# Kernel optimization log

Measured on AMD Instinct MI355X. Metric: run time of the kernel, lower is better.

Reference implementation:

```python
import jax, jax.numpy as jnp
import numpy as np

N = 50000        # nodes
E = 1_600_000    # edges
F = 32           # in/out channels
T = 4            # towers
FT = F // T      # per-tower channels = 8
ED = 16          # edge_dim
L = 5            # num PNA layers


def setup_inputs() -> dict:
    key = jax.random.key(0)
    ks = jax.random.split(key, 11)
    s = 0.2  # weight scale
    return {
        "x": jax.random.normal(ks[0], (N, F), jnp.float32),
        "edge_index": jax.random.randint(ks[1], (2, E), 0, N, dtype=jnp.int32),
        "edge_attr": jax.random.normal(ks[2], (E, ED), jnp.float32),
        # per-layer stacked PNAConv parameters
        "edge_W": jax.random.normal(ks[3], (L, ED, FT), jnp.float32) * s,
        "edge_b": jax.random.normal(ks[4], (L, FT), jnp.float32) * s,
        "pre_W": jax.random.normal(ks[5], (L, T, 3 * FT, FT), jnp.float32) * s,
        "pre_b": jax.random.normal(ks[6], (L, T, FT), jnp.float32) * s,
        "post_W": jax.random.normal(ks[7], (L, T, 4 * FT, FT), jnp.float32) * s,
        "post_b": jax.random.normal(ks[8], (L, T, FT), jnp.float32) * s,
        "lin_W": jax.random.normal(ks[9], (L, T * FT, F), jnp.float32) * s,
        "lin_b": jax.random.normal(ks[10], (L, F), jnp.float32) * s,
    }


def _pna_layer(x, src, dst, edge_attr, eW, eb, pW, pb, poW, pob, lW, lb):
    n = x.shape[0]
    xt = x.reshape(n, T, FT)                       # divide_input=True
    ee = edge_attr @ eW + eb                       # [E, FT], shared edge encoder
    xi = xt[dst]                                   # target node features [E, T, FT]
    xj = xt[src]                                   # source node features [E, T, FT]
    ee_b = jnp.broadcast_to(ee[:, None, :], (ee.shape[0], T, FT))
    h = jnp.concatenate([xi, xj, ee_b], axis=-1)   # [E, T, 3*FT]
    # per-tower pre-MLP (pre_layers=1)
    h = jnp.einsum('etk,tkf->etf', h, pW) + pb     # [E, T, FT]
    # aggregators: mean, sum, max (scaler = identity)
    ssum = jax.ops.segment_sum(h, dst, num_segments=n)
    cnt = jax.ops.segment_sum(jnp.ones((h.shape[0],), h.dtype), dst, num_segments=n)
    mean = ssum / jnp.maximum(cnt, 1.0)[:, None, None]
    mx = jax.ops.segment_max(h, dst, num_segments=n)
    mx = jnp.where(cnt[:, None, None] > 0, mx, 0.0)  # empty segments -> 0 (PyG convention)
    out = jnp.concatenate([xt, mean, ssum, mx], axis=-1)  # [N, T, 4*FT]
    # per-tower post-MLP (post_layers=1)
    out = jnp.einsum('ntk,tkf->ntf', out, poW) + pob      # [N, T, FT]
    out = out.reshape(n, T * FT) @ lW + lb                # final mixing linear
    return jax.nn.relu(out)


def reference(x, edge_index, edge_attr, edge_W, edge_b, pre_W, pre_b,
              post_W, post_b, lin_W, lin_b):
    src, dst = edge_index[0], edge_index[1]
    for l in range(L):
        x = _pna_layer(x, src, dst, edge_attr,
                       edge_W[l], edge_b[l], pre_W[l], pre_b[l],
                       post_W[l], post_b[l], lin_W[l], lin_b[l])
    return x
```

## Files before the change

### kernel.cpp

```cpp
#include <hip/hip_runtime.h>
#include <hip/hip_fp16.h>

#define NN 50000
#define NE 1600000
#define F 32
#define T 4
#define FT 8
#define ED 16
#define NLAYERS 5

typedef _Float16 h2 __attribute__((ext_vector_type(2)));

__device__ __forceinline__ float dot2(h2 a, h2 b, float c) {
#if __has_builtin(__builtin_amdgcn_fdot2)
    return __builtin_amdgcn_fdot2(a, b, c, false);
#else
    return c + (float)a.x * (float)b.x + (float)a.y * (float)b.y;
#endif
}

#if __has_builtin(__builtin_amdgcn_global_load_lds)
#define HAS_GLDS 1
__device__ __forceinline__ void glds16(const void* g, void* l) {
    __builtin_amdgcn_global_load_lds(
        (const __attribute__((address_space(1))) unsigned*)g,
        (__attribute__((address_space(3))) unsigned*)l, 16, 0, 0);
}
__device__ __forceinline__ void glds4(const void* g, void* l) {
    __builtin_amdgcn_global_load_lds(
        (const __attribute__((address_space(1))) unsigned*)g,
        (__attribute__((address_space(3))) unsigned*)l, 4, 0, 0);
}
#endif


__global__ void zero_cnt(int* __restrict__ cnt) {
    int i = blockIdx.x * 256 + threadIdx.x;
    if (i < NN) cnt[i] = 0;
}

__global__ void count_kernel(const int* __restrict__ ei, int* __restrict__ cnt) {
    int e = blockIdx.x * 256 + threadIdx.x;
    if (e >= NE) return;
    atomicAdd(&cnt[ei[NE + e]], 1);
}

__global__ void scan_kernel(const int* __restrict__ cnt, int* __restrict__ row_ptr,
                            int* __restrict__ cursor) {
    __shared__ int wsum[16];
    __shared__ int carry_s;
    int tid = threadIdx.x;
    int lane = tid & 63, wid = tid >> 6;
    if (tid == 0) carry_s = 0;
    __syncthreads();
    for (int base = 0; base < NN; base += 1024) {
        int i = base + tid;
        int v = (i < NN) ? cnt[i] : 0;
        int s = v;
#pragma unroll
        for (int off = 1; off < 64; off <<= 1) {
            int tt = __shfl_up(s, off, 64);
            if (lane >= off) s += tt;
        }
        __syncthreads();
        if (lane == 63) wsum[wid] = s;
        __syncthreads();
        if (wid == 0 && lane < 16) {
            int w = wsum[lane];
            int ws = w;
#pragma unroll
            for (int off = 1; off < 16; off <<= 1) {
                int tt = __shfl_up(ws, off, 16);
                if (lane >= off) ws += tt;
            }
            wsum[lane] = ws - w;
        }
        __syncthreads();
        int excl = carry_s + wsum[wid] + s - v;
        if (i < NN) { row_ptr[i] = excl; cursor[i] = excl; }
        __syncthreads();
        if (tid == 1023) carry_s += wsum[15] + s;
    }
}

__global__ void build_kernel(const int* __restrict__ ei,
                             const float* __restrict__ eattr,
                             int* __restrict__ cursor,
                             int* __restrict__ src_s,
                             float4* __restrict__ eh) {
    int e = blockIdx.x * 256 + threadIdx.x;
    if (e >= NE) return;
    int src = ei[e];
    int dst = ei[NE + e];
    const float4* eap = (const float4*)(eattr + (size_t)e * ED);
    float4 v0 = eap[0], v1 = eap[1], v2 = eap[2], v3 = eap[3];
    union { __half hh[16]; float4 f4[2]; } u;
    u.hh[0]  = __float2half(v0.x); u.hh[1]  = __float2half(v0.y);
    u.hh[2]  = __float2half(v0.z); u.hh[3]  = __float2half(v0.w);
    u.hh[4]  = __float2half(v1.x); u.hh[5]  = __float2half(v1.y);
    u.hh[6]  = __float2half(v1.z); u.hh[7]  = __float2half(v1.w);
    u.hh[8]  = __float2half(v2.x); u.hh[9]  = __float2half(v2.y);
    u.hh[10] = __float2half(v2.z); u.hh[11] = __float2half(v2.w);
    u.hh[12] = __float2half(v3.x); u.hh[13] = __float2half(v3.y);
    u.hh[14] = __float2half(v3.z); u.hh[15] = __float2half(v3.w);
    int p = atomicAdd(&cursor[dst], 1);
    src_s[p] = src << 5;
    eh[2 * (size_t)p]     = u.f4[0];
    eh[2 * (size_t)p + 1] = u.f4[1];
}

__global__ void layer_const(const float* __restrict__ edge_W,
                            const float* __restrict__ edge_b,
                            const float* __restrict__ pre_W,
                            const float* __restrict__ pre_b,
                            float4* __restrict__ wchp,
                            float* __restrict__ abias) {
    int idx = threadIdx.x;
    if (idx >= NLAYERS * 32) return;
    int l = idx >> 5, ch = idx & 31;
    int t = ch >> 3, f = ch & 7;
    const float* eW = edge_W + (size_t)l * ED * FT;
    const float* eb = edge_b + (size_t)l * FT;
    const float* pW = pre_W + (size_t)l * T * 24 * FT;
    const float* pb = pre_b + (size_t)l * T * FT;
    float pj[8];
#pragma unroll
    for (int j = 0; j < 8; j++) pj[j] = pW[(t * 24 + 16 + j) * 8 + f];
    union { _Float16 hh[16]; float4 f4[2]; } u;
#pragma unroll
    for (int k = 0; k < 16; k++) {
        float s = 0.f;
#pragma unroll
        for (int j = 0; j < 8; j++) s += eW[k * 8 + j] * pj[j];
        u.hh[k] = (_Float16)s;
    }
    float c0 = pb[t * 8 + f];
#pragma unroll
    for (int j = 0; j < 8; j++) c0 += eb[j] * pj[j];
    wchp[2 * idx]     = u.f4[0];
    wchp[2 * idx + 1] = u.f4[1];
    abias[idx] = c0;
}


__device__ __forceinline__ unsigned short f2bf_rne(float v) {
    unsigned u = __float_as_uint(v);
    return (unsigned short)((u + 0x7FFFu + ((u >> 16) & 1u)) >> 16);
}

__global__ void node_pre(const float* __restrict__ xin,
                         const float* __restrict__ preW,
                         unsigned short* __restrict__ b16) {
    int idx = blockIdx.x * 256 + threadIdx.x;
    if (idx >= NN * F) return;
    int n = idx >> 5, ch = idx & 31;
    int t = ch >> 3, f = ch & 7;
    const float* xrow = xin + n * F + t * FT;
    const float* wB = preW + (t * 24 + 8) * 8 + f;
    float bv = 0.f;
#pragma unroll
    for (int k = 0; k < 8; k++) bv += xrow[k] * wB[k * 8];
    b16[idx] = f2bf_rne(bv);
}

__global__ __launch_bounds__(256) void gather_post(
        const float* __restrict__ xin,
        const unsigned short* __restrict__ b16_in,
        unsigned short* __restrict__ b16_out,
        const float4* __restrict__ eh,
        const int* __restrict__ row_ptr, const int* __restrict__ cnt,
        const int* __restrict__ src_s,
        const float4* __restrict__ wchp_l,
        const float* __restrict__ abias_l,
        const float* __restrict__ preW,
        const float* __restrict__ postW, const float* __restrict__ postb,
        const float* __restrict__ linW, const float* __restrict__ linb,
        const float* __restrict__ preW_next,
        float* __restrict__ xout) {
    __shared__ __align__(16) char stage[4][2304];
    __shared__ float smS[4][32];
    __shared__ float smM[4][32];
    int tid = threadIdx.x;
    int wv = tid >> 6;
    int lane = tid & 63;
    int n = blockIdx.x * 4 + wv;

    int chgrp = lane >> 3;
    int e_sub = lane & 7;
    const unsigned short* bp = b16_in + chgrp * 4;

    union { float4 f4[8]; h2 p[32]; } uw;
#pragma unroll
    for (int c = 0; c < 4; c++) {
        uw.f4[2 * c]     = wchp_l[2 * (chgrp * 4 + c)];
        uw.f4[2 * c + 1] = wchp_l[2 * (chgrp * 4 + c) + 1];
    }

    int rs = row_ptr[n], deg = cnt[n];
    int re = rs + deg;
    float xv = xin[(size_t)n * F + (lane & 31)];

    char* ehbuf = stage[wv];
    const int* srcbuf = (const int*)(stage[wv] + 2048);

    float S[4] = {0.f, 0.f, 0.f, 0.f};
    float M[4] = {-3.4e38f, -3.4e38f, -3.4e38f, -3.4e38f};
    const unsigned MAXS = (NN - 1) * F;

    for (int base = rs; base < re; base += 64) {
        const char* ehb = (const char*)(eh + 2 * (size_t)base);
#ifdef HAS_GLDS
        glds16(ehb + lane * 16, ehbuf);
        glds16(ehb + 1024 + lane * 16, ehbuf + 1024);
        glds4((const char*)(src_s + base) + lane * 4, (void*)srcbuf);
        asm volatile("s_waitcnt vmcnt(0)" ::: "memory");
#else
        *(float4*)(ehbuf + lane * 16) = *(const float4*)(ehb + lane * 16);
        *(float4*)(ehbuf + 1024 + lane * 16) = *(const float4*)(ehb + 1024 + lane * 16);
        ((int*)srcbuf)[lane] = src_s[base + lane];
#endif
        ushort4 bk[8];
#pragma unroll
        for (int k = 0; k < 8; k++) {
            unsigned s = (unsigned)srcbuf[e_sub + 8 * k];
            if (s > MAXS) s = 0;
            bk[k] = *(const ushort4*)(bp + s);
        }
#pragma unroll
        for (int k = 0; k < 8; k++) {
            int j = e_sub + 8 * k;
            bool valid = (base + j) < re;
            union { float4 f4; h2 p[4]; } ua, ub;
            ua.f4 = *(const float4*)(ehbuf + j * 32);
            ub.f4 = *(const float4*)(ehbuf + j * 32 + 16);
            unsigned short bvv[4] = {bk[k].x, bk[k].y, bk[k].z, bk[k].w};
#pragma unroll
            for (int c = 0; c < 4; c++) {
                float h = __uint_as_float((unsigned)bvv[c] << 16);
                h = dot2(ua.p[0], uw.p[c * 8 + 0], h);
                h = dot2(ua.p[1], uw.p[c * 8 + 1], h);
                h = dot2(ua.p[2], uw.p[c * 8 + 2], h);
                h = dot2(ua.p[3], uw.p[c * 8 + 3], h);
                h = dot2(ub.p[0], uw.p[c * 8 + 4], h);
                h = dot2(ub.p[1], uw.p[c * 8 + 5], h);
                h = dot2(ub.p[2], uw.p[c * 8 + 6], h);
                h = dot2(ub.p[3], uw.p[c * 8 + 7], h);
                S[c] += valid ? h : 0.f;
                M[c] = valid ? fmaxf(M[c], h) : M[c];
            }
        }
    }
#pragma unroll
    for (int m = 1; m < 8; m <<= 1) {
#pragma unroll
        for (int c = 0; c < 4; c++) {
            S[c] += __shfl_xor(S[c], m, 64);
            M[c] = fmaxf(M[c], __shfl_xor(M[c], m, 64));
        }
    }
    if (e_sub == 0) {
#pragma unroll
        for (int c = 0; c < 4; c++) {
            smS[wv][chgrp * 4 + c] = S[c];
            smM[wv][chgrp * 4 + c] = M[c];
        }
    }
    __syncthreads();

    int ch = lane & 31, half = lane >> 5;
    int t = ch >> 3, f = ch & 7;
    float Sc = smS[wv][ch];
    float Mc = smM[wv][ch];

    float a_val = abias_l[ch];
#pragma unroll
    for (int j = 0; j < 8; j++)
        a_val += __shfl(xv, t * 8 + j, 64) * preW[(t * 24 + j) * 8 + f];

    float sum_h, mean_h, max_h;
    if (deg > 0) {
        sum_h = Sc + (float)deg * a_val;
        mean_h = sum_h / (float)deg;
        max_h = Mc + a_val;
    } else {
        sum_h = 0.f; mean_h = 0.f; max_h = 0.f;
    }

    float ua0 = 0.f, ua1 = 0.f, ua2 = 0.f, ua3 = 0.f;
#pragma unroll
    for (int kk = 0; kk < 8; kk++) {
        int sl = t * 8 + kk;
        ua0 += __shfl(xv,     sl, 64) * postW[(t * 32 + 0 * 8 + kk) * 8 + f];
        ua1 += __shfl(mean_h, sl, 64) * postW[(t * 32 + 1 * 8 + kk) * 8 + f];
        ua2 += __shfl(sum_h,  sl, 64) * postW[(t * 32 + 2 * 8 + kk) * 8 + f];
        ua3 += __shfl(max_h,  sl, 64) * postW[(t * 32 + 3 * 8 + kk) * 8 + f];
    }
    float u2 = postb[t * 8 + f] + ((ua0 + ua1) + (ua2 + ua3));

    float y0 = 0.f, y1 = 0.f, y2 = 0.f, y3 = 0.f;
#pragma unroll
    for (int k = 0; k < 8; k++) {
        y0 += __shfl(u2, k,      64) * linW[k * 32 + ch];
        y1 += __shfl(u2, 8 + k,  64) * linW[(8 + k) * 32 + ch];
        y2 += __shfl(u2, 16 + k, 64) * linW[(16 + k) * 32 + ch];
        y3 += __shfl(u2, 24 + k, 64) * linW[(24 + k) * 32 + ch];
    }
    float y = linb[ch] + ((y0 + y1) + (y2 + y3));
    y = fmaxf(y, 0.f);
    if (half == 0)
        xout[(size_t)n * F + ch] = y;

    if (preW_next) {
        float bn = 0.f;
#pragma unroll
        for (int j = 0; j < 8; j++)
            bn += __shfl(y, t * 8 + j, 64) * preW_next[(t * 24 + 8 + j) * 8 + f];
        if (half == 0)
            b16_out[(size_t)n * F + ch] = f2bf_rne(bn);
    }
}


extern "C" void kernel_launch(void* const* d_in, const int* in_sizes, int n_in,
                              void* d_out, int out_size, void* d_ws, size_t ws_size,
                              hipStream_t stream) {
    const float* x      = (const float*)d_in[0];
    const int*   ei     = (const int*)d_in[1];
    const float* eattr  = (const float*)d_in[2];
    const float* edge_W = (const float*)d_in[3];
    const float* edge_b = (const float*)d_in[4];
    const float* pre_W  = (const float*)d_in[5];
    const float* pre_b  = (const float*)d_in[6];
    const float* post_W = (const float*)d_in[7];
    const float* post_b = (const float*)d_in[8];
    const float* lin_W  = (const float*)d_in[9];
    const float* lin_b  = (const float*)d_in[10];
    float* out = (float*)d_out;

    const size_t NC = (size_t)NN * F;
    char* p = (char*)d_ws;
    float4* eh    = (float4*)p;        p += sizeof(float4) * 2 * (size_t)NE;
    int* src_s    = (int*)p;           p += sizeof(int) * NE;
    int* cnt      = (int*)p;           p += sizeof(int) * NN;
    int* row_ptr  = (int*)p;           p += sizeof(int) * NN;
    int* cursor   = (int*)p;           p += sizeof(int) * NN;
    unsigned short* b16a = (unsigned short*)p;  p += sizeof(unsigned short) * NC;
    unsigned short* b16b = (unsigned short*)p;  p += sizeof(unsigned short) * NC;
    float* xb0    = (float*)p;         p += sizeof(float) * NC;
    float* xb1    = (float*)p;         p += sizeof(float) * NC;
    float4* wchp  = (float4*)p;        p += sizeof(float4) * 2 * NLAYERS * 32;
    float* abias  = (float*)p;         p += sizeof(float) * NLAYERS * 32;

    dim3 blk(256);
    int gN  = (NN + 255) / 256;
    int gE  = (NE + 255) / 256;
    int gNC = (NN * F + 255) / 256;
    int gG  = NN / 4;

    hipLaunchKernelGGL(zero_cnt,     dim3(gN), blk, 0, stream, cnt);
    hipLaunchKernelGGL(count_kernel, dim3(gE), blk, 0, stream, ei, cnt);
    hipLaunchKernelGGL(scan_kernel,  dim3(1), dim3(1024), 0, stream, cnt, row_ptr, cursor);
    hipLaunchKernelGGL(build_kernel, dim3(gE), blk, 0, stream, ei, eattr,
                       cursor, src_s, eh);
    hipLaunchKernelGGL(layer_const,  dim3(1), blk, 0, stream,
                       edge_W, edge_b, pre_W, pre_b, wchp, abias);

    hipLaunchKernelGGL(node_pre, dim3(gNC), blk, 0, stream, x, pre_W, b16a);

    const float* xin = x;
    for (int l = 0; l < NLAYERS; l++) {
        const float* pW  = pre_W  + (size_t)l * T * 24 * FT;
        const float* poW = post_W + (size_t)l * T * 32 * FT;
        const float* pob = post_b + (size_t)l * T * FT;
        const float* lW  = lin_W  + (size_t)l * F * F;
        const float* lb  = lin_b  + (size_t)l * F;
        const float* pWn = (l + 1 < NLAYERS) ? (pre_W + (size_t)(l + 1) * T * 24 * FT)
                                             : nullptr;
        float* xout = (l == NLAYERS - 1) ? out : ((l & 1) ? xb1 : xb0);
        const unsigned short* bin  = (l & 1) ? b16b : b16a;
        unsigned short*       bout = (l & 1) ? b16a : b16b;

        hipLaunchKernelGGL(gather_post, dim3(gG), blk, 0, stream,
                           xin, bin, pWn ? bout : nullptr, eh, row_ptr, cnt, src_s,
                           wchp + (size_t)l * 64, abias + (size_t)l * 32,
                           pW, poW, pob, lW, lb, pWn, xout);
        xin = xout;
    }
}
```

Measured before the change: 744.9 us.

## Sort nodes by degree, double-buffer edge staging, and narrow lane channel groups

Adds a degree histogram and counting sort so each block's four waves handle nodes of similar degree, which reduces per-block imbalance. The gather loop now processes edges in chunks of 32 with double-buffered async global-to-LDS loads, prefetching the next chunk while the current one is computed. Each lane now covers 2 channels across 4 edge sub-lanes instead of 4 channels across 8, cutting registers and the shuffle-reduction depth. In exchange it adds three small preprocessing kernels, an indirection for node ids, and a scattered write order for outputs.

```diff
diff --git a/kernel.cpp b/kernel.cpp
--- a/kernel.cpp
+++ b/kernel.cpp
@@ -34,9 +34,10 @@
 #endif
 
 
-__global__ void zero_cnt(int* __restrict__ cnt) {
+__global__ void zero_cnt(int* __restrict__ cnt, int* __restrict__ dhist) {
     int i = blockIdx.x * 256 + threadIdx.x;
     if (i < NN) cnt[i] = 0;
+    if (blockIdx.x == 0 && threadIdx.x < 256) dhist[threadIdx.x] = 0;
 }
 
 __global__ void count_kernel(const int* __restrict__ ei, int* __restrict__ cnt) {
@@ -81,6 +82,29 @@
         __syncthreads();
         if (tid == 1023) carry_s += wsum[15] + s;
     }
+}
+
+__global__ void hist_kernel(const int* __restrict__ cnt, int* __restrict__ dhist) {
+    int n = blockIdx.x * 256 + threadIdx.x;
+    if (n >= NN) return;
+    int d = cnt[n]; if (d > 255) d = 255;
+    atomicAdd(&dhist[d], 1);
+}
+
+__global__ void scan_hist(const int* __restrict__ dhist, int* __restrict__ dcur) {
+    if (threadIdx.x == 0) {
+        int acc = 0;
+        for (int i = 0; i < 256; i++) { dcur[i] = acc; acc += dhist[i]; }
+    }
+}
+
+__global__ void order_kernel(const int* __restrict__ cnt, int* __restrict__ dcur,
+                             int* __restrict__ node_order) {
+    int n = blockIdx.x * 256 + threadIdx.x;
+    if (n >= NN) return;
+    int d = cnt[n]; if (d > 255) d = 255;
+    int pos = atomicAdd(&dcur[d], 1);
+    node_order[pos] = n;
 }
 
 __global__ void build_kernel(const int* __restrict__ ei,
@@ -170,6 +194,7 @@
         const float4* __restrict__ eh,
         const int* __restrict__ row_ptr, const int* __restrict__ cnt,
         const int* __restrict__ src_s,
+        const int* __restrict__ node_order,
         const float4* __restrict__ wchp_l,
         const float* __restrict__ abias_l,
         const float* __restrict__ preW,
@@ -183,87 +208,107 @@
     int tid = threadIdx.x;
     int wv = tid >> 6;
     int lane = tid & 63;
-    int n = blockIdx.x * 4 + wv;
-
-    int chgrp = lane >> 3;
-    int e_sub = lane & 7;
-    const unsigned short* bp = b16_in + chgrp * 4;
-
-    union { float4 f4[8]; h2 p[32]; } uw;
-#pragma unroll
-    for (int c = 0; c < 4; c++) {
-        uw.f4[2 * c]     = wchp_l[2 * (chgrp * 4 + c)];
-        uw.f4[2 * c + 1] = wchp_l[2 * (chgrp * 4 + c) + 1];
-    }
+    int n = node_order[blockIdx.x * 4 + wv];
+
+    int chgrp = lane >> 2;
+    int e_sub = lane & 3;
+    const unsigned short* bp = b16_in + chgrp * 2;
+
+    union { float4 f4[4]; h2 p[16]; } uw;
+    uw.f4[0] = wchp_l[2 * (chgrp * 2)];
+    uw.f4[1] = wchp_l[2 * (chgrp * 2) + 1];
+    uw.f4[2] = wchp_l[2 * (chgrp * 2 + 1)];
+    uw.f4[3] = wchp_l[2 * (chgrp * 2 + 1) + 1];
 
     int rs = row_ptr[n], deg = cnt[n];
     int re = rs + deg;
+    int nch = (deg + 31) >> 5;
     float xv = xin[(size_t)n * F + (lane & 31)];
 
-    char* ehbuf = stage[wv];
-    const int* srcbuf = (const int*)(stage[wv] + 2048);
-
-    float S[4] = {0.f, 0.f, 0.f, 0.f};
-    float M[4] = {-3.4e38f, -3.4e38f, -3.4e38f, -3.4e38f};
+    char* stw = stage[wv];
     const unsigned MAXS = (NN - 1) * F;
 
-    for (int base = rs; base < re; base += 64) {
-        const char* ehb = (const char*)(eh + 2 * (size_t)base);
+    float S0 = 0.f, S1 = 0.f, M0 = -3.4e38f, M1 = -3.4e38f;
+
 #ifdef HAS_GLDS
-        glds16(ehb + lane * 16, ehbuf);
-        glds16(ehb + 1024 + lane * 16, ehbuf + 1024);
-        glds4((const char*)(src_s + base) + lane * 4, (void*)srcbuf);
+    {
+        const char* ehg = (const char*)(eh + 2 * (size_t)rs);
+        glds16(ehg + lane * 16, stw);
+        if (lane < 32) glds4((const char*)(src_s + rs) + lane * 4, stw + 2048);
+    }
+    for (int c = 0; c < nch; ++c) {
+        int base = rs + c * 32;
+        const char* eb = stw + (c & 1) * 1024;
+        const int* sb = (const int*)(stw + 2048 + (c & 1) * 128);
         asm volatile("s_waitcnt vmcnt(0)" ::: "memory");
-#else
-        *(float4*)(ehbuf + lane * 16) = *(const float4*)(ehb + lane * 16);
-        *(float4*)(ehbuf + 1024 + lane * 16) = *(const float4*)(ehb + 1024 + lane * 16);
-        ((int*)srcbuf)[lane] = src_s[base + lane];
-#endif
-        ushort4 bk[8];
+        __builtin_amdgcn_sched_barrier(0);
+        ushort2 bk[8];
 #pragma unroll
         for (int k = 0; k < 8; k++) {
-            unsigned s = (unsigned)srcbuf[e_sub + 8 * k];
+            unsigned s = (unsigned)sb[e_sub + 4 * k];
             if (s > MAXS) s = 0;
-            bk[k] = *(const ushort4*)(bp + s);
+            bk[k] = *(const ushort2*)(bp + s);
         }
+        __builtin_amdgcn_sched_barrier(0);
+        int nxt = (c + 1 < nch) ? base + 32 : base;
+        const char* ehgn = (const char*)(eh + 2 * (size_t)nxt);
+        char* ebn = stw + ((c + 1) & 1) * 1024;
+        glds16(ehgn + lane * 16, ebn);
+        if (lane < 32) glds4((const char*)(src_s + nxt) + lane * 4,
+                             stw + 2048 + ((c + 1) & 1) * 128);
+        __builtin_amdgcn_sched_barrier(0);
 #pragma unroll
         for (int k = 0; k < 8; k++) {
-            int j = e_sub + 8 * k;
+            int j = e_sub + 4 * k;
             bool valid = (base + j) < re;
             union { float4 f4; h2 p[4]; } ua, ub;
-            ua.f4 = *(const float4*)(ehbuf + j * 32);
-            ub.f4 = *(const float4*)(ehbuf + j * 32 + 16);
-            unsigned short bvv[4] = {bk[k].x, bk[k].y, bk[k].z, bk[k].w};
-#pragma unroll
-            for (int c = 0; c < 4; c++) {
-                float h = __uint_as_float((unsigned)bvv[c] << 16);
-                h = dot2(ua.p[0], uw.p[c * 8 + 0], h);
-                h = dot2(ua.p[1], uw.p[c * 8 + 1], h);
-                h = dot2(ua.p[2], uw.p[c * 8 + 2], h);
-                h = dot2(ua.p[3], uw.p[c * 8 + 3], h);
-                h = dot2(ub.p[0], uw.p[c * 8 + 4], h);
-                h = dot2(ub.p[1], uw.p[c * 8 + 5], h);
-                h = dot2(ub.p[2], uw.p[c * 8 + 6], h);
-                h = dot2(ub.p[3], uw.p[c * 8 + 7], h);
-                S[c] += valid ? h : 0.f;
-                M[c] = valid ? fmaxf(M[c], h) : M[c];
-            }
+            ua.f4 = *(const float4*)(eb + j * 32);
+            ub.f4 = *(const float4*)(eb + j * 32 + 16);
+            float h0 = __uint_as_float((unsigned)bk[k].x << 16);
+            float h1 = __uint_as_float((unsigned)bk[k].y << 16);
+            h0 = dot2(ua.p[0], uw.p[0], h0);  h1 = dot2(ua.p[0], uw.p[8],  h1);
+            h0 = dot2(ua.p[1], uw.p[1], h0);  h1 = dot2(ua.p[1], uw.p[9],  h1);
+            h0 = dot2(ua.p[2], uw.p[2], h0);  h1 = dot2(ua.p[2], uw.p[10], h1);
+            h0 = dot2(ua.p[3], uw.p[3], h0);  h1 = dot2(ua.p[3], uw.p[11], h1);
+            h0 = dot2(ub.p[0], uw.p[4], h0);  h1 = dot2(ub.p[0], uw.p[12], h1);
+            h0 = dot2(ub.p[1], uw.p[5], h0);  h1 = dot2(ub.p[1], uw.p[13], h1);
+            h0 = dot2(ub.p[2], uw.p[6], h0);  h1 = dot2(ub.p[2], uw.p[14], h1);
+            h0 = dot2(ub.p[3], uw.p[7], h0);  h1 = dot2(ub.p[3], uw.p[15], h1);
+            S0 += valid ? h0 : 0.f;
+            S1 += valid ? h1 : 0.f;
+            M0 = valid ? fmaxf(M0, h0) : M0;
+            M1 = valid ? fmaxf(M1, h1) : M1;
         }
     }
-#pragma unroll
-    for (int m = 1; m < 8; m <<= 1) {
-#pragma unroll
-        for (int c = 0; c < 4; c++) {
-            S[c] += __shfl_xor(S[c], m, 64);
-            M[c] = fmaxf(M[c], __shfl_xor(M[c], m, 64));
+#else
+    for (int i = rs + e_sub; i < re; i += 4) {
+        unsigned s = (unsigned)src_s[i];
+        union { float4 f4; h2 p[4]; } ua, ub;
+        ua.f4 = eh[2 * (size_t)i]; ub.f4 = eh[2 * (size_t)i + 1];
+        ushort2 b2v = *(const ushort2*)(bp + s);
+        float h0 = __uint_as_float((unsigned)b2v.x << 16);
+        float h1 = __uint_as_float((unsigned)b2v.y << 16);
+#pragma unroll
+        for (int q = 0; q < 4; q++) {
+            h0 = dot2(ua.p[q], uw.p[q], h0);     h1 = dot2(ua.p[q], uw.p[8 + q], h1);
+            h0 = dot2(ub.p[q], uw.p[4 + q], h0); h1 = dot2(ub.p[q], uw.p[12 + q], h1);
         }
+        S0 += h0; S1 += h1;
+        M0 = fmaxf(M0, h0); M1 = fmaxf(M1, h1);
+    }
+#endif
+#pragma unroll
+    for (int m = 1; m < 4; m <<= 1) {
+        S0 += __shfl_xor(S0, m, 64);
+        S1 += __shfl_xor(S1, m, 64);
+        M0 = fmaxf(M0, __shfl_xor(M0, m, 64));
+        M1 = fmaxf(M1, __shfl_xor(M1, m, 64));
     }
     if (e_sub == 0) {
-#pragma unroll
-        for (int c = 0; c < 4; c++) {
-            smS[wv][chgrp * 4 + c] = S[c];
-            smM[wv][chgrp * 4 + c] = M[c];
-        }
+        smS[wv][chgrp * 2]     = S0;
+        smS[wv][chgrp * 2 + 1] = S1;
+        smM[wv][chgrp * 2]     = M0;
+        smM[wv][chgrp * 2 + 1] = M1;
     }
     __syncthreads();
 
@@ -344,6 +389,9 @@
     int* cnt      = (int*)p;           p += sizeof(int) * NN;
     int* row_ptr  = (int*)p;           p += sizeof(int) * NN;
     int* cursor   = (int*)p;           p += sizeof(int) * NN;
+    int* node_order = (int*)p;         p += sizeof(int) * NN;
+    int* dhist    = (int*)p;           p += sizeof(int) * 256;
+    int* dcur     = (int*)p;           p += sizeof(int) * 256;
     unsigned short* b16a = (unsigned short*)p;  p += sizeof(unsigned short) * NC;
     unsigned short* b16b = (unsigned short*)p;  p += sizeof(unsigned short) * NC;
     float* xb0    = (float*)p;         p += sizeof(float) * NC;
@@ -357,11 +405,14 @@
     int gNC = (NN * F + 255) / 256;
     int gG  = NN / 4;
 
-    hipLaunchKernelGGL(zero_cnt,     dim3(gN), blk, 0, stream, cnt);
+    hipLaunchKernelGGL(zero_cnt,     dim3(gN), blk, 0, stream, cnt, dhist);
     hipLaunchKernelGGL(count_kernel, dim3(gE), blk, 0, stream, ei, cnt);
     hipLaunchKernelGGL(scan_kernel,  dim3(1), dim3(1024), 0, stream, cnt, row_ptr, cursor);
     hipLaunchKernelGGL(build_kernel, dim3(gE), blk, 0, stream, ei, eattr,
                        cursor, src_s, eh);
+    hipLaunchKernelGGL(hist_kernel,  dim3(gN), blk, 0, stream, cnt, dhist);
+    hipLaunchKernelGGL(scan_hist,    dim3(1), dim3(64), 0, stream, dhist, dcur);
+    hipLaunchKernelGGL(order_kernel, dim3(gN), blk, 0, stream, cnt, dcur, node_order);
     hipLaunchKernelGGL(layer_const,  dim3(1), blk, 0, stream,
                        edge_W, edge_b, pre_W, pre_b, wchp, abias);
 
@@ -382,7 +433,7 @@
 
         hipLaunchKernelGGL(gather_post, dim3(gG), blk, 0, stream,
                            xin, bin, pWn ? bout : nullptr, eh, row_ptr, cnt, src_s,
-                           wchp + (size_t)l * 64, abias + (size_t)l * 32,
+                           node_order, wchp + (size_t)l * 64, abias + (size_t)l * 32,
                            pW, poW, pob, lW, lb, pWn, xout);
         xin = xout;
     }
```

Result: slower. 823.2 us (+10.5%).
